# Performance work log

Measured on AMD Instinct MI355X. Metric: run time of the kernel, lower is better.

The kernel has to match this reference:

```python
import jax, jax.numpy as jnp
import numpy as np
import math

B, S, D_IN, D_Q = 4, 2048, 512, 512

def setup_inputs() -> dict:
    key = jax.random.key(0)
    ks = jax.random.split(key, 7)
    s_in = 1.0 / math.sqrt(D_IN)
    x = jax.random.normal(ks[0], (B, S, D_IN), dtype=jnp.float32)
    # nn.Linear-style params: W [out,in], b [out]; uniform(-1/sqrt(in), 1/sqrt(in))
    Wq = jax.random.uniform(ks[1], (D_Q, D_IN), jnp.float32, -s_in, s_in)
    bq = jax.random.uniform(ks[2], (D_Q,), jnp.float32, -s_in, s_in)
    Wk = jax.random.uniform(ks[3], (D_Q, D_IN), jnp.float32, -s_in, s_in)
    bk = jax.random.uniform(ks[4], (D_Q,), jnp.float32, -s_in, s_in)
    Wv = jax.random.uniform(ks[5], (D_Q, D_IN), jnp.float32, -s_in, s_in)
    bv = jax.random.uniform(ks[6], (D_Q,), jnp.float32, -s_in, s_in)
    return {"x": x, "Wq": Wq, "bq": bq, "Wk": Wk, "bk": bk, "Wv": Wv, "bv": bv}

def reference(x, Wq, bq, Wk, bk, Wv, bv):
    # Q/K/V projections: [B,S,D_IN] @ W^T + b -> [B,S,D_Q]
    Q = jnp.einsum('bsi,qi->bsq', x, Wq) + bq
    K = jnp.einsum('bsi,qi->bsq', x, Wk) + bk
    V = jnp.einsum('bsi,qi->bsq', x, Wv) + bv
    scale = 1.0 / math.sqrt(D_Q)
    scores = jnp.einsum('bsq,btq->bst', Q, K) * scale  # [B,S,S]
    attention = jax.nn.softmax(scores, axis=-1)        # 'atten_prob'
    weighted = jnp.einsum('bst,btq->bsq', attention, V)  # 'atten_score'
    return (attention, weighted)
```

## Files before the change

kernel.cpp:

```cpp
#include <hip/hip_runtime.h>
#include <hip/hip_bf16.h>

typedef unsigned short u16;
typedef short bf16x8 __attribute__((ext_vector_type(8)));
typedef float f32x4 __attribute__((ext_vector_type(4)));

#define S_LEN 2048
#define DQ 512
#define NBATCH 4

__device__ __forceinline__ u16 f2bf(float f) {
    __hip_bfloat16 h = __float2bfloat16(f);
    return *reinterpret_cast<u16*>(&h);
}
__device__ __forceinline__ float bf2f(u16 u) {
    unsigned v = ((unsigned)u) << 16;
    union { unsigned u; float f; } c; c.u = v; return c.f;
}

__device__ __forceinline__ void async16(const u16* g, u16* l) {
    __builtin_amdgcn_global_load_lds(
        (__attribute__((address_space(1))) void*)g,
        (__attribute__((address_space(3))) void*)l, 16, 0, 0);
}

__device__ __forceinline__ int xcd_swz(int bid, int chunk) {
    return (bid & 7) * chunk + (bid >> 3);
}

__global__ __launch_bounds__(256) void k_cvt_all(const float* __restrict__ x,
                                                 const float* __restrict__ wq,
                                                 const float* __restrict__ wk,
                                                 const float* __restrict__ wv,
                                                 u16* __restrict__ xb, u16* __restrict__ wb,
                                                 float* __restrict__ sums) {
    int bid = blockIdx.x;
    if (bid >= 4864) {
        int i = (bid - 4864) * 256 + threadIdx.x;
        *(f32x4*)(sums + (size_t)i * 4) = (f32x4)0.0f;
        return;
    }
    const float* src;
    u16* dst;
    int i;
    if (bid < 4096)      { src = x;  dst = xb;          i = bid * 256 + threadIdx.x; }
    else if (bid < 4352) { src = wq; dst = wb;          i = (bid - 4096) * 256 + threadIdx.x; }
    else if (bid < 4608) { src = wk; dst = wb + 262144; i = (bid - 4352) * 256 + threadIdx.x; }
    else                 { src = wv; dst = wb + 524288; i = (bid - 4608) * 256 + threadIdx.x; }
    f32x4 v = *(const f32x4*)(src + (size_t)i * 4);
    ushort4 o;
    o.x = f2bf(v.x); o.y = f2bf(v.y); o.z = f2bf(v.z); o.w = f2bf(v.w);
    *(ushort4*)(dst + (size_t)i * 4) = o;
}

__device__ __forceinline__ void gemm_core(const u16* __restrict__ A, const u16* __restrict__ B,
                                          int lda, int ldb, int kend,
                                          f32x4 acc[4][4], u16* ldsA, u16* ldsB, int tid) {
    const int lane = tid & 63;
    const int w    = tid >> 6;
    const int wm   = (w & 1) << 6;
    const int wn   = (w >> 1) << 6;
    const int l16  = lane & 15;
    const int quad = lane >> 4;

    for (int k0 = 0; k0 < kend; k0 += 32) {
#pragma unroll
        for (int i = 0; i < 2; ++i) {
            int c  = i * 256 + tid;
            int r  = c >> 2;
            int cc = (c & 3) << 3;
            async16(A + (size_t)r * lda + k0 + cc, ldsA + r * 32 + cc);
            async16(B + (size_t)r * ldb + k0 + cc, ldsB + r * 32 + cc);
        }
        __syncthreads();
        bf16x8 af[4], bf[4];
#pragma unroll
        for (int i = 0; i < 4; ++i)
            af[i] = *(const bf16x8*)(ldsA + (wm + i * 16 + l16) * 32 + quad * 8);
#pragma unroll
        for (int j = 0; j < 4; ++j)
            bf[j] = *(const bf16x8*)(ldsB + (wn + j * 16 + l16) * 32 + quad * 8);
#pragma unroll
        for (int i = 0; i < 4; ++i)
#pragma unroll
            for (int j = 0; j < 4; ++j)
                acc[i][j] = __builtin_amdgcn_mfma_f32_16x16x32_bf16(af[i], bf[j], acc[i][j], 0, 0, 0);
        __syncthreads();
    }
}

__global__ __launch_bounds__(256) void k_proj(const u16* __restrict__ xb, const u16* __restrict__ Wb,
                                              const float* __restrict__ bq, const float* __restrict__ bk,
                                              const float* __restrict__ bv, u16* __restrict__ out,
                                              u16* __restrict__ VT) {
    __shared__ __align__(16) u16 lds[8192];
    const int l  = xcd_swz(blockIdx.x, 96);
    const int bx = l & 3;
    const int by = (l >> 2) & 63;
    const int z  = l >> 8;
    const int m0 = by * 128, n0 = bx * 128;
    const u16* A = xb + (size_t)m0 * DQ;
    const u16* B = Wb + (size_t)z * DQ * DQ + (size_t)n0 * DQ;
    const float* bias = (z == 0) ? bq : (z == 1) ? bk : bv;

    f32x4 acc[4][4];
#pragma unroll
    for (int i = 0; i < 4; ++i)
#pragma unroll
        for (int j = 0; j < 4; ++j) acc[i][j] = (f32x4)0.0f;

    int tid = threadIdx.x;
    gemm_core(A, B, DQ, DQ, DQ, acc, lds, lds + 4096, tid);

    const int lane = tid & 63, w = tid >> 6;
    const int wm = (w & 1) << 6, wn = (w >> 1) << 6;
    const int l16 = lane & 15, quad = lane >> 4;

    if (z < 2) {
        u16* outz = out + (size_t)z * 8192 * DQ;
#pragma unroll
        for (int j = 0; j < 4; ++j) {
            int gn = n0 + wn + j * 16 + l16;
            float bb = bias[gn];
#pragma unroll
            for (int i = 0; i < 4; ++i)
#pragma unroll
                for (int r = 0; r < 4; ++r) {
                    int gm = m0 + wm + i * 16 + quad * 4 + r;
                    outz[(size_t)gm * DQ + gn] = f2bf(acc[i][j][r] + bb);
                }
        }
    } else {
        const int b = m0 >> 11;
        u16* VTb_ = VT + (size_t)b * DQ * S_LEN;
#pragma unroll
        for (int j = 0; j < 4; ++j) {
            int gn = n0 + wn + j * 16 + l16;
            float bb = bias[gn];
#pragma unroll
            for (int i = 0; i < 4; ++i) {
                int t0 = (m0 & 2047) + wm + i * 16 + quad * 4;
                ushort4 o;
                o.x = f2bf(acc[i][j][0] + bb);
                o.y = f2bf(acc[i][j][1] + bb);
                o.z = f2bf(acc[i][j][2] + bb);
                o.w = f2bf(acc[i][j][3] + bb);
                *(ushort4*)(VTb_ + (size_t)gn * S_LEN + t0) = o;
            }
        }
    }
}

__global__ __launch_bounds__(256) void k_scores(const u16* __restrict__ Qb, const u16* __restrict__ Kb,
                                                u16* __restrict__ Pb, float* __restrict__ sums) {
    __shared__ __align__(16) u16 lds[8192];
    const int l  = xcd_swz(blockIdx.x, 128);
    const int bx = l & 15;
    const int by = (l >> 4) & 15;
    const int b  = l >> 8;
    const int m0 = by * 128, n0 = bx * 128;
    const u16* A = Qb + ((size_t)b * S_LEN + m0) * DQ;
    const u16* B = Kb + ((size_t)b * S_LEN + n0) * DQ;

    f32x4 acc[4][4];
#pragma unroll
    for (int i = 0; i < 4; ++i)
#pragma unroll
        for (int j = 0; j < 4; ++j) acc[i][j] = (f32x4)0.0f;

    int tid = threadIdx.x;
    gemm_core(A, B, DQ, DQ, DQ, acc, lds, lds + 4096, tid);

    const float scale = 0.044194173824159216f;
    const int lane = tid & 63, w = tid >> 6;
    const int wm = (w & 1) << 6, wn = (w >> 1) << 6;
    const int l16 = lane & 15, quad = lane >> 4;
    u16* prow = Pb + (size_t)(b * S_LEN + m0) * S_LEN;

    float psum[4][4];
#pragma unroll
    for (int i = 0; i < 4; ++i)
#pragma unroll
        for (int r = 0; r < 4; ++r) psum[i][r] = 0.0f;

#pragma unroll
    for (int i = 0; i < 4; ++i)
#pragma unroll
        for (int j = 0; j < 4; ++j)
#pragma unroll
            for (int r = 0; r < 4; ++r) {
                int gm = wm + i * 16 + quad * 4 + r;
                int gn = n0 + wn + j * 16 + l16;
                float e = __expf(acc[i][j][r] * scale);
                u16 pb = f2bf(e);
                prow[(size_t)gm * S_LEN + gn] = pb;
                psum[i][r] += bf2f(pb);
            }

    float* sums_row = sums + b * S_LEN + m0;
#pragma unroll
    for (int i = 0; i < 4; ++i)
#pragma unroll
        for (int r = 0; r < 4; ++r) {
            float v = psum[i][r];
            v += __shfl_xor(v, 1);
            v += __shfl_xor(v, 2);
            v += __shfl_xor(v, 4);
            v += __shfl_xor(v, 8);
            if (l16 == 0) atomicAdd(&sums_row[wm + i * 16 + quad * 4 + r], v);
        }
}

__global__ __launch_bounds__(256) void k_pv(const u16* __restrict__ Pb, const u16* __restrict__ VT,
                                            const float* __restrict__ sums,
                                            float* __restrict__ probs,
                                            float* __restrict__ wout) {
    __shared__ __align__(16) u16 lds[12288];
    u16* ldsA = lds;
    u16* ldsB = lds + 8192;
    const int l  = xcd_swz(blockIdx.x, 64);
    const int bx = l & 7;
    const int by = (l >> 3) & 15;
    const int b  = l >> 7;
    const int m0 = by * 128, n0 = bx * 64;
    const u16* A = Pb + (size_t)(b * S_LEN + m0) * S_LEN;
    const u16* B = VT + (size_t)b * DQ * S_LEN + (size_t)n0 * S_LEN;

    const int tid  = threadIdx.x;
    const int lane = tid & 63;
    const int w    = tid >> 6;
    const int wm   = (w & 1) << 6;
    const int wn   = (w >> 1) << 5;
    const int l16  = lane & 15;
    const int quad = lane >> 4;

    f32x4 acc[4][2];
#pragma unroll
    for (int i = 0; i < 4; ++i)
#pragma unroll
        for (int j = 0; j < 2; ++j) acc[i][j] = (f32x4)0.0f;

    for (int k0 = 0; k0 < S_LEN; k0 += 64) {
#pragma unroll
        for (int h = 0; h < 2; ++h) {
#pragma unroll
            for (int it = 0; it < 2; ++it) {
                int c  = it * 256 + tid;
                int r  = c >> 2;
                int cc = (c & 3) << 3;
                async16(A + (size_t)r * S_LEN + k0 + h * 32 + cc, ldsA + h * 4096 + r * 32 + cc);
            }
            {
                int r  = tid >> 2;
                int cc = (tid & 3) << 3;
                async16(B + (size_t)r * S_LEN + k0 + h * 32 + cc, ldsB + h * 2048 + r * 32 + cc);
            }
        }
        __syncthreads();
        bf16x8 af[2][4], bfr[2][2];
#pragma unroll
        for (int h = 0; h < 2; ++h) {
#pragma unroll
            for (int i = 0; i < 4; ++i)
                af[h][i] = *(const bf16x8*)(ldsA + h * 4096 + (wm + i * 16 + l16) * 32 + quad * 8);
#pragma unroll
            for (int j = 0; j < 2; ++j)
                bfr[h][j] = *(const bf16x8*)(ldsB + h * 2048 + (wn + j * 16 + l16) * 32 + quad * 8);
        }
#pragma unroll
        for (int h = 0; h < 2; ++h)
#pragma unroll
            for (int i = 0; i < 4; ++i)
#pragma unroll
                for (int j = 0; j < 2; ++j)
                    acc[i][j] = __builtin_amdgcn_mfma_f32_16x16x32_bf16(af[h][i], bfr[h][j], acc[i][j], 0, 0, 0);
        __syncthreads();
    }

    float* ldsInv = (float*)lds;
    if (tid < 128) ldsInv[tid] = 1.0f / sums[b * S_LEN + m0 + tid];
    __syncthreads();

    float* outb = wout + (size_t)b * S_LEN * DQ;
#pragma unroll
    for (int i = 0; i < 4; ++i) {
#pragma unroll
        for (int r = 0; r < 4; ++r) {
            int lm = wm + i * 16 + quad * 4 + r;
            float inv = ldsInv[lm];
#pragma unroll
            for (int j = 0; j < 2; ++j) {
                int gn = n0 + wn + j * 16 + l16;
                outb[(size_t)(m0 + lm) * DQ + gn] = acc[i][j][r] * inv;
            }
        }
    }

    const u16* Psl = Pb + (size_t)(b * S_LEN + m0) * S_LEN + bx * 256;
    float* Pro = probs + ((size_t)b * S_LEN + m0) * S_LEN + bx * 256;
#pragma unroll
    for (int it = 0; it < 16; ++it) {
        int idx = it * 256 + tid;
        int r  = idx >> 5;
        int cc = (idx & 31) << 3;
        float inv = ldsInv[r];
        bf16x8 vv = *(const bf16x8*)(Psl + (size_t)r * S_LEN + cc);
        f32x4 o0, o1;
        o0.x = bf2f((u16)vv[0]) * inv;
        o0.y = bf2f((u16)vv[1]) * inv;
        o0.z = bf2f((u16)vv[2]) * inv;
        o0.w = bf2f((u16)vv[3]) * inv;
        o1.x = bf2f((u16)vv[4]) * inv;
        o1.y = bf2f((u16)vv[5]) * inv;
        o1.z = bf2f((u16)vv[6]) * inv;
        o1.w = bf2f((u16)vv[7]) * inv;
        float* dst = Pro + (size_t)r * S_LEN + cc;
        *(f32x4*)(dst) = o0;
        *(f32x4*)(dst + 4) = o1;
    }
}

extern "C" void kernel_launch(void* const* d_in, const int* in_sizes, int n_in,
                              void* d_out, int out_size, void* d_ws, size_t ws_size,
                              hipStream_t stream) {
    const float* x  = (const float*)d_in[0];
    const float* Wq = (const float*)d_in[1];
    const float* bq = (const float*)d_in[2];
    const float* Wk = (const float*)d_in[3];
    const float* bk = (const float*)d_in[4];
    const float* Wv = (const float*)d_in[5];
    const float* bv = (const float*)d_in[6];

    char* ws = (char*)d_ws;
    u16* xb  = (u16*)(ws);
    u16* Wb  = (u16*)(ws + 8388608);
    u16* Qb  = (u16*)(ws + 9961472);
    u16* Kb  = (u16*)(ws + 18350080);
    u16* VTb = (u16*)(ws + 35127296);
    u16* Pb  = (u16*)(ws + 43515904);
    float* sums = (float*)(ws + 77070336);
    float* probs = (float*)d_out;
    float* wout  = (float*)d_out + 16777216;

    k_cvt_all<<<4872, 256, 0, stream>>>(x, Wq, Wk, Wv, xb, Wb, sums);
    k_proj<<<768, 256, 0, stream>>>(xb, Wb, bq, bk, bv, Qb, VTb);
    k_scores<<<1024, 256, 0, stream>>>(Qb, Kb, Pb, sums);
    k_pv<<<512, 256, 0, stream>>>(Pb, VTb, sums, probs, wout);
}
```

Before: 203.2 us.

## Use 256x256 double-buffered swizzled-LDS GEMM for projection and score kernels

Replaces the 128x128 single-buffered GEMM core with a 256x256 tile over 512 threads (8 waves), a 64-wide K step, XOR-swizzled LDS layout and double buffering. Async global-to-LDS prefetch of the next K slice is interleaved between MFMA groups, and s_setprio is raised around the MFMA groups. The aim is to hide load latency, cut LDS bank conflicts and reuse more data per tile. In exchange the kernels need 128KB of LDS per block and launch far fewer blocks (192 and 256), so occupancy and load balance across CUs drop.

Measured after the change: 193.0 us. -5.0%, faster.

```diff
diff --git a/kernel.cpp b/kernel.cpp
--- a/kernel.cpp
+++ b/kernel.cpp
@@ -53,153 +53,232 @@
     *(ushort4*)(dst + (size_t)i * 4) = o;
 }
 
-__device__ __forceinline__ void gemm_core(const u16* __restrict__ A, const u16* __restrict__ B,
-                                          int lda, int ldb, int kend,
-                                          f32x4 acc[4][4], u16* ldsA, u16* ldsB, int tid) {
+__device__ __forceinline__ void stage_unit(const u16* __restrict__ G, u16* buf,
+                                           int kcol, int h, int tid) {
+#pragma unroll
+    for (int q = 0; q < 2; ++q) {
+        int c   = q * 512 + tid;
+        int r   = c >> 3;
+        int p   = c & 7;
+        int lch = p ^ (r & 7);
+        async16(G + (size_t)(h * 128 + r) * DQ + kcol + lch * 8,
+                buf + h * 8192 + c * 8);
+    }
+}
+
+__device__ __forceinline__ void gemm256(const u16* __restrict__ A, const u16* __restrict__ B,
+                                        u16* ldsA, u16* ldsB, f32x4 acc[8][4], int tid) {
     const int lane = tid & 63;
     const int w    = tid >> 6;
-    const int wm   = (w & 1) << 6;
-    const int wn   = (w >> 1) << 6;
+    const int wr   = w >> 2;
+    const int wc   = w & 3;
     const int l16  = lane & 15;
     const int quad = lane >> 4;
-
-    for (int k0 = 0; k0 < kend; k0 += 32) {
-#pragma unroll
-        for (int i = 0; i < 2; ++i) {
-            int c  = i * 256 + tid;
-            int r  = c >> 2;
-            int cc = (c & 3) << 3;
-            async16(A + (size_t)r * lda + k0 + cc, ldsA + r * 32 + cc);
-            async16(B + (size_t)r * ldb + k0 + cc, ldsB + r * 32 + cc);
-        }
+    const int p0   = quad ^ (l16 & 7);
+    const int a0   = (wr * 128 + l16) * 64 + p0 * 8;
+    const int a1   = (wr * 128 + l16) * 64 + (p0 ^ 4) * 8;
+    const int b0   = (wc * 64 + l16) * 64 + p0 * 8;
+    const int b1   = (wc * 64 + l16) * 64 + (p0 ^ 4) * 8;
+
+    stage_unit(A, ldsA, 0, 0, tid);
+    stage_unit(A, ldsA, 0, 1, tid);
+    stage_unit(B, ldsB, 0, 0, tid);
+    stage_unit(B, ldsB, 0, 1, tid);
+    __syncthreads();
+
+    for (int kt = 0; kt < 8; ++kt) {
+        const u16* rdA = ldsA + (kt & 1) * 16384;
+        const u16* rdB = ldsB + (kt & 1) * 16384;
+        u16* wrA = ldsA + ((kt + 1) & 1) * 16384;
+        u16* wrB = ldsB + ((kt + 1) & 1) * 16384;
+        const int  kc = (kt + 1) * 64;
+        const bool pf = kt < 7;
+        bf16x8 a[4][2], bbf[2][2];
+
+        if (pf) stage_unit(A, wrA, kc, 0, tid);
+#pragma unroll
+        for (int i = 0; i < 4; ++i) {
+            a[i][0] = *(const bf16x8*)(rdA + a0 + i * 1024);
+            a[i][1] = *(const bf16x8*)(rdA + a1 + i * 1024);
+        }
+#pragma unroll
+        for (int j = 0; j < 2; ++j) {
+            bbf[j][0] = *(const bf16x8*)(rdB + b0 + j * 1024);
+            bbf[j][1] = *(const bf16x8*)(rdB + b1 + j * 1024);
+        }
+        __builtin_amdgcn_s_setprio(1);
+#pragma unroll
+        for (int i = 0; i < 4; ++i)
+#pragma unroll
+            for (int j = 0; j < 2; ++j) {
+                acc[i][j] = __builtin_amdgcn_mfma_f32_16x16x32_bf16(a[i][0], bbf[j][0], acc[i][j], 0, 0, 0);
+                acc[i][j] = __builtin_amdgcn_mfma_f32_16x16x32_bf16(a[i][1], bbf[j][1], acc[i][j], 0, 0, 0);
+            }
+        __builtin_amdgcn_s_setprio(0);
+
+        if (pf) stage_unit(A, wrA, kc, 1, tid);
+#pragma unroll
+        for (int j = 0; j < 2; ++j) {
+            bbf[j][0] = *(const bf16x8*)(rdB + b0 + (2 + j) * 1024);
+            bbf[j][1] = *(const bf16x8*)(rdB + b1 + (2 + j) * 1024);
+        }
+        __builtin_amdgcn_s_setprio(1);
+#pragma unroll
+        for (int i = 0; i < 4; ++i)
+#pragma unroll
+            for (int j = 0; j < 2; ++j) {
+                acc[i][2 + j] = __builtin_amdgcn_mfma_f32_16x16x32_bf16(a[i][0], bbf[j][0], acc[i][2 + j], 0, 0, 0);
+                acc[i][2 + j] = __builtin_amdgcn_mfma_f32_16x16x32_bf16(a[i][1], bbf[j][1], acc[i][2 + j], 0, 0, 0);
+            }
+        __builtin_amdgcn_s_setprio(0);
+
+        if (pf) stage_unit(B, wrB, kc, 0, tid);
+#pragma unroll
+        for (int i = 0; i < 4; ++i) {
+            a[i][0] = *(const bf16x8*)(rdA + a0 + (4 + i) * 1024);
+            a[i][1] = *(const bf16x8*)(rdA + a1 + (4 + i) * 1024);
+        }
+        __builtin_amdgcn_s_setprio(1);
+#pragma unroll
+        for (int i = 0; i < 4; ++i)
+#pragma unroll
+            for (int j = 0; j < 2; ++j) {
+                acc[4 + i][2 + j] = __builtin_amdgcn_mfma_f32_16x16x32_bf16(a[i][0], bbf[j][0], acc[4 + i][2 + j], 0, 0, 0);
+                acc[4 + i][2 + j] = __builtin_amdgcn_mfma_f32_16x16x32_bf16(a[i][1], bbf[j][1], acc[4 + i][2 + j], 0, 0, 0);
+            }
+        __builtin_amdgcn_s_setprio(0);
+
+        if (pf) stage_unit(B, wrB, kc, 1, tid);
+#pragma unroll
+        for (int j = 0; j < 2; ++j) {
+            bbf[j][0] = *(const bf16x8*)(rdB + b0 + j * 1024);
+            bbf[j][1] = *(const bf16x8*)(rdB + b1 + j * 1024);
+        }
+        __builtin_amdgcn_s_setprio(1);
+#pragma unroll
+        for (int i = 0; i < 4; ++i)
+#pragma unroll
+            for (int j = 0; j < 2; ++j) {
+                acc[4 + i][j] = __builtin_amdgcn_mfma_f32_16x16x32_bf16(a[i][0], bbf[j][0], acc[4 + i][j], 0, 0, 0);
+                acc[4 + i][j] = __builtin_amdgcn_mfma_f32_16x16x32_bf16(a[i][1], bbf[j][1], acc[4 + i][j], 0, 0, 0);
+            }
+        __builtin_amdgcn_s_setprio(0);
+
         __syncthreads();
-        bf16x8 af[4], bf[4];
-#pragma unroll
-        for (int i = 0; i < 4; ++i)
-            af[i] = *(const bf16x8*)(ldsA + (wm + i * 16 + l16) * 32 + quad * 8);
-#pragma unroll
-        for (int j = 0; j < 4; ++j)
-            bf[j] = *(const bf16x8*)(ldsB + (wn + j * 16 + l16) * 32 + quad * 8);
-#pragma unroll
-        for (int i = 0; i < 4; ++i)
-#pragma unroll
-            for (int j = 0; j < 4; ++j)
-                acc[i][j] = __builtin_amdgcn_mfma_f32_16x16x32_bf16(af[i], bf[j], acc[i][j], 0, 0, 0);
-        __syncthreads();
-    }
-}
-
-__global__ __launch_bounds__(256) void k_proj(const u16* __restrict__ xb, const u16* __restrict__ Wb,
-                                              const float* __restrict__ bq, const float* __restrict__ bk,
-                                              const float* __restrict__ bv, u16* __restrict__ out,
-                                              u16* __restrict__ VT) {
-    __shared__ __align__(16) u16 lds[8192];
-    const int l  = xcd_swz(blockIdx.x, 96);
-    const int bx = l & 3;
-    const int by = (l >> 2) & 63;
-    const int z  = l >> 8;
-    const int m0 = by * 128, n0 = bx * 128;
+    }
+}
+
+__global__ __launch_bounds__(512, 2) void k_proj(const u16* __restrict__ xb, const u16* __restrict__ Wb,
+                                                 const float* __restrict__ bq, const float* __restrict__ bk,
+                                                 const float* __restrict__ bv, u16* __restrict__ out,
+                                                 u16* __restrict__ VT) {
+    __shared__ __align__(16) u16 lds[65536];
+    const int l  = xcd_swz(blockIdx.x, 24);
+    const int bx = l & 1;
+    const int by = (l >> 1) & 31;
+    const int z  = l >> 6;
+    const int m0 = by * 256, n0 = bx * 256;
     const u16* A = xb + (size_t)m0 * DQ;
     const u16* B = Wb + (size_t)z * DQ * DQ + (size_t)n0 * DQ;
     const float* bias = (z == 0) ? bq : (z == 1) ? bk : bv;
 
-    f32x4 acc[4][4];
-#pragma unroll
-    for (int i = 0; i < 4; ++i)
+    f32x4 acc[8][4];
+#pragma unroll
+    for (int i = 0; i < 8; ++i)
 #pragma unroll
         for (int j = 0; j < 4; ++j) acc[i][j] = (f32x4)0.0f;
 
-    int tid = threadIdx.x;
-    gemm_core(A, B, DQ, DQ, DQ, acc, lds, lds + 4096, tid);
+    const int tid = threadIdx.x;
+    gemm256(A, B, lds, lds + 32768, acc, tid);
 
     const int lane = tid & 63, w = tid >> 6;
-    const int wm = (w & 1) << 6, wn = (w >> 1) << 6;
+    const int wr = w >> 2, wc = w & 3;
     const int l16 = lane & 15, quad = lane >> 4;
 
     if (z < 2) {
         u16* outz = out + (size_t)z * 8192 * DQ;
 #pragma unroll
         for (int j = 0; j < 4; ++j) {
-            int gn = n0 + wn + j * 16 + l16;
-            float bb = bias[gn];
-#pragma unroll
-            for (int i = 0; i < 4; ++i)
+            int gn = n0 + wc * 64 + j * 16 + l16;
+            float bv_ = bias[gn];
+#pragma unroll
+            for (int i = 0; i < 8; ++i)
 #pragma unroll
                 for (int r = 0; r < 4; ++r) {
-                    int gm = m0 + wm + i * 16 + quad * 4 + r;
-                    outz[(size_t)gm * DQ + gn] = f2bf(acc[i][j][r] + bb);
+                    int gm = m0 + wr * 128 + i * 16 + quad * 4 + r;
+                    outz[(size_t)gm * DQ + gn] = f2bf(acc[i][j][r] + bv_);
                 }
         }
     } else {
-        const int b = m0 >> 11;
-        u16* VTb_ = VT + (size_t)b * DQ * S_LEN;
+        const int bb_ = m0 >> 11;
+        u16* VTb_ = VT + (size_t)bb_ * DQ * S_LEN;
 #pragma unroll
         for (int j = 0; j < 4; ++j) {
-            int gn = n0 + wn + j * 16 + l16;
-            float bb = bias[gn];
-#pragma unroll
-            for (int i = 0; i < 4; ++i) {
-                int t0 = (m0 & 2047) + wm + i * 16 + quad * 4;
+            int gn = n0 + wc * 64 + j * 16 + l16;
+            float bv_ = bias[gn];
+#pragma unroll
+            for (int i = 0; i < 8; ++i) {
+                int t0 = (m0 & 2047) + wr * 128 + i * 16 + quad * 4;
                 ushort4 o;
-                o.x = f2bf(acc[i][j][0] + bb);
-                o.y = f2bf(acc[i][j][1] + bb);
-                o.z = f2bf(acc[i][j][2] + bb);
-                o.w = f2bf(acc[i][j][3] + bb);
+                o.x = f2bf(acc[i][j][0] + bv_);
+                o.y = f2bf(acc[i][j][1] + bv_);
+                o.z = f2bf(acc[i][j][2] + bv_);
+                o.w = f2bf(acc[i][j][3] + bv_);
                 *(ushort4*)(VTb_ + (size_t)gn * S_LEN + t0) = o;
             }
         }
     }
 }
 
-__global__ __launch_bounds__(256) void k_scores(const u16* __restrict__ Qb, const u16* __restrict__ Kb,
-                                                u16* __restrict__ Pb, float* __restrict__ sums) {
-    __shared__ __align__(16) u16 lds[8192];
-    const int l  = xcd_swz(blockIdx.x, 128);
-    const int bx = l & 15;
-    const int by = (l >> 4) & 15;
-    const int b  = l >> 8;
-    const int m0 = by * 128, n0 = bx * 128;
+__global__ __launch_bounds__(512, 2) void k_scores(const u16* __restrict__ Qb, const u16* __restrict__ Kb,
+                                                   u16* __restrict__ Pb, float* __restrict__ sums) {
+    __shared__ __align__(16) u16 lds[65536];
+    const int l  = xcd_swz(blockIdx.x, 32);
+    const int bx = l & 7;
+    const int by = (l >> 3) & 7;
+    const int b  = l >> 6;
+    const int m0 = by * 256, n0 = bx * 256;
     const u16* A = Qb + ((size_t)b * S_LEN + m0) * DQ;
     const u16* B = Kb + ((size_t)b * S_LEN + n0) * DQ;
 
-    f32x4 acc[4][4];
-#pragma unroll
-    for (int i = 0; i < 4; ++i)
+    f32x4 acc[8][4];
+#pragma unroll
+    for (int i = 0; i < 8; ++i)
 #pragma unroll
         for (int j = 0; j < 4; ++j) acc[i][j] = (f32x4)0.0f;
 
-    int tid = threadIdx.x;
-    gemm_core(A, B, DQ, DQ, DQ, acc, lds, lds + 4096, tid);
+    const int tid = threadIdx.x;
+    gemm256(A, B, lds, lds + 32768, acc, tid);
 
     const float scale = 0.044194173824159216f;
     const int lane = tid & 63, w = tid >> 6;
-    const int wm = (w & 1) << 6, wn = (w >> 1) << 6;
+    const int wr = w >> 2, wc = w & 3;
     const int l16 = lane & 15, quad = lane >> 4;
     u16* prow = Pb + (size_t)(b * S_LEN + m0) * S_LEN;
 
-    float psum[4][4];
-#pragma unroll
-    for (int i = 0; i < 4; ++i)
+    float psum[8][4];
+#pragma unroll
+    for (int i = 0; i < 8; ++i)
 #pragma unroll
         for (int r = 0; r < 4; ++r) psum[i][r] = 0.0f;
 
 #pragma unroll
-    for (int i = 0; i < 4; ++i)
+    for (int i = 0; i < 8; ++i)
 #pragma unroll
         for (int j = 0; j < 4; ++j)
 #pragma unroll
             for (int r = 0; r < 4; ++r) {
-                int gm = wm + i * 16 + quad * 4 + r;
-                int gn = n0 + wn + j * 16 + l16;
+                int gm = wr * 128 + i * 16 + quad * 4 + r;
+                int gn = n0 + wc * 64 + j * 16 + l16;
                 float e = __expf(acc[i][j][r] * scale);
-                u16 pb = f2bf(e);
-                prow[(size_t)gm * S_LEN + gn] = pb;
-                psum[i][r] += bf2f(pb);
-            }
-
-    float* sums_row = sums + b * S_LEN + m0;
-#pragma unroll
-    for (int i = 0; i < 4; ++i)
+                u16 pbv = f2bf(e);
+                prow[(size_t)gm * S_LEN + gn] = pbv;
+                psum[i][r] += bf2f(pbv);
+            }
+
+    float* sums_row = sums + b * S_LEN + m0 + wr * 128;
+#pragma unroll
+    for (int i = 0; i < 8; ++i)
 #pragma unroll
         for (int r = 0; r < 4; ++r) {
             float v = psum[i][r];
@@ -207,7 +286,7 @@
             v += __shfl_xor(v, 2);
             v += __shfl_xor(v, 4);
             v += __shfl_xor(v, 8);
-            if (l16 == 0) atomicAdd(&sums_row[wm + i * 16 + quad * 4 + r], v);
+            if (l16 == 0) atomicAdd(&sums_row[i * 16 + quad * 4 + r], v);
         }
 }
 
@@ -343,7 +422,7 @@
     float* wout  = (float*)d_out + 16777216;
 
     k_cvt_all<<<4872, 256, 0, stream>>>(x, Wq, Wk, Wv, xb, Wb, sums);
-    k_proj<<<768, 256, 0, stream>>>(xb, Wb, bq, bk, bv, Qb, VTb);
-    k_scores<<<1024, 256, 0, stream>>>(Qb, Kb, Pb, sums);
+    k_proj<<<192, 512, 0, stream>>>(xb, Wb, bq, bk, bv, Qb, VTb);
+    k_scores<<<256, 512, 0, stream>>>(Qb, Kb, Pb, sums);
     k_pv<<<512, 256, 0, stream>>>(Pb, VTb, sums, probs, wout);
 }
```
